# Kernel optimization log

Hardware: AMD Instinct MI355X
Metric: run time of the kernel (lower is better)

The kernel has to match this reference:

```python
import jax, jax.numpy as jnp
import numpy as np

N = 100000
E = 1600000
K = 15        # kernel_size (num Gaussian mixture components)
DIM = 3       # pseudo-coordinate dim
EPS = 1e-15   # PyG GMMConv sigma epsilon
BN_EPS = 1e-5
CH = [(50, 75), (75, 100), (100, 75), (75, 50)]


def setup_inputs() -> dict:
    key = jax.random.key(0)
    ks = iter(jax.random.split(key, 64))
    inp = {}
    inp["x"] = jax.random.normal(next(ks), (N, 50), jnp.float32)
    inp["edge_index"] = jax.random.randint(next(ks), (2, E), 0, N, jnp.int64)
    inp["edge_attr"] = jax.random.uniform(next(ks), (E, DIM), jnp.float32)
    for l, (cin, cout) in enumerate(CH, 1):
        inp[f"g{l}"] = jax.random.normal(next(ks), (cin, K, cout), jnp.float32) * 0.1
        inp[f"mu{l}"] = jax.random.normal(next(ks), (K, DIM), jnp.float32)
        inp[f"sigma{l}"] = jnp.ones((K, DIM), jnp.float32) + 0.1 * jax.random.uniform(next(ks), (K, DIM), jnp.float32)
        inp[f"root{l}"] = jax.random.normal(next(ks), (cin, cout), jnp.float32) * 0.1
        inp[f"b{l}"] = jax.random.normal(next(ks), (cout,), jnp.float32) * 0.01
        if l < 4:
            inp[f"gamma{l}"] = jnp.ones((cout,), jnp.float32)
            inp[f"beta{l}"] = jnp.zeros((cout,), jnp.float32)
    return inp


def gmm_layer(x, src, tgt, pseudo, g, mu, sigma, root, bias):
    # Gaussian mixture edge weights: w[e,k] = exp(-0.5 * sum_d (u_ed - mu_kd)^2 / sigma_kd^2)
    n = x.shape[0]
    diff = pseudo[:, None, :] - mu[None, :, :]              # [E,K,dim]
    w = jnp.exp(-0.5 * jnp.sum(diff * diff / (sigma[None] ** 2 + EPS), axis=-1))  # [E,K]
    xs = x[src]                                             # gather source feats [E,Cin]
    # out_t = sum_k (sum_{e->t} w_ek * x_src[e]) @ G_k  (avoids [E,K,Cout] tensor)
    agg = jnp.zeros((n, g.shape[2]), x.dtype)
    for k in range(K):
        zk = jax.ops.segment_sum(xs * w[:, k:k + 1], tgt, num_segments=n)  # [N,Cin]
        agg = agg + zk @ g[:, k, :]
    deg = jax.ops.segment_sum(jnp.ones((src.shape[0],), x.dtype), tgt, num_segments=n)
    agg = agg / jnp.maximum(deg, 1.0)[:, None]              # aggr='mean'
    return agg + x @ root + bias


def batchnorm(x, gamma, beta):
    m = jnp.mean(x, axis=0)
    v = jnp.var(x, axis=0)
    return gamma * (x - m) * jax.lax.rsqrt(v + BN_EPS) + beta


def reference(x, edge_index, edge_attr,
              g1, mu1, sigma1, root1, b1, gamma1, beta1,
              g2, mu2, sigma2, root2, b2, gamma2, beta2,
              g3, mu3, sigma3, root3, b3, gamma3, beta3,
              g4, mu4, sigma4, root4, b4):
    src, tgt = edge_index[0], edge_index[1]
    h = jax.nn.elu(gmm_layer(x, src, tgt, edge_attr, g1, mu1, sigma1, root1, b1))
    h = batchnorm(h, gamma1, beta1)
    h = jax.nn.elu(gmm_layer(h, src, tgt, edge_attr, g2, mu2, sigma2, root2, b2))
    h = batchnorm(h, gamma2, beta2)
    h = jax.nn.elu(gmm_layer(h, src, tgt, edge_attr, g3, mu3, sigma3, root3, b3))
    h = batchnorm(h, gamma3, beta3)
    return gmm_layer(h, src, tgt, edge_attr, g4, mu4, sigma4, root4, b4)
```

## Files before the change

kernel.cpp:

```cpp
#include <hip/hip_runtime.h>
#include <stdint.h>

#define NN 100000
#define NE 1600000
#define KG 15

typedef unsigned short u16;
typedef __attribute__((ext_vector_type(8))) short short8;
typedef __attribute__((ext_vector_type(4))) short short4_t;
typedef __attribute__((ext_vector_type(8))) __bf16 bf16x8;
typedef __attribute__((ext_vector_type(4))) float f32x4;

#ifdef __has_builtin
# if __has_builtin(__builtin_amdgcn_mfma_f32_16x16x16bf16_1k)
#  define HAS_MFMA16 1
# endif
#endif
#ifndef HAS_MFMA16
# define HAS_MFMA16 0
#endif

static __device__ __forceinline__ float bf2f(u16 u){ return __uint_as_float(((unsigned)u)<<16); }
static __device__ __forceinline__ u16 f2bf(float f){
  unsigned u = __float_as_uint(f);
  u += 0x7FFFu + ((u>>16)&1u);
  return (u16)(u>>16);
}
static __device__ __forceinline__ float ldf(const void* p, long long i, int isf32){
  return isf32 ? ((const float*)p)[i] : bf2f(((const u16*)p)[i]);
}
static __device__ __forceinline__ int ld_idx(const void* p, long long i, int isi64){
  return isi64 ? (int)((const long long*)p)[i] : ((const int*)p)[i];
}
static __device__ __forceinline__ f32x4 mfma16x16x32(short8 a, short8 b, f32x4 c){
  return __builtin_amdgcn_mfma_f32_16x16x32_bf16(
      __builtin_bit_cast(bf16x8, a), __builtin_bit_cast(bf16x8, b), c, 0, 0, 0);
}
#if HAS_MFMA16
static __device__ __forceinline__ f32x4 mfma16x16x16(short4_t a, short4_t b, f32x4 c){
  return __builtin_amdgcn_mfma_f32_16x16x16bf16_1k(a, b, c, 0, 0, 0);
}
#endif

__global__ void k_sentinel(float* out, float val){
  if (threadIdx.x == 0 && blockIdx.x == 0) out[0] = val;
}

__global__ void k_probe(const void* sg1, const void* ei, int* flags){
  if (threadIdx.x == 0 && blockIdx.x == 0){
    const u16* p = (const u16*)sg1;
    int sane = 1;
    for (int i=0;i<45;i++){ float v = bf2f(p[i]); if (!(v > 0.5f && v < 2.0f)) sane = 0; }
    flags[0] = sane ? 0 : 1;
    const int* q = (const int*)ei;
    int allz = 1;
    for (int i=1;i<128;i+=2) if (q[i] != 0) allz = 0;
    flags[1] = allz ? 1 : 0;
  }
}

__global__ __launch_bounds__(256) void k_convx(const void* x, u16* xcv, const int* flags){
  int i = blockIdx.x*256 + threadIdx.x;
  int c = i & 63, r = i >> 6;
  if (r >= NN) return;
  int isf = flags[0];
  u16 v = 0;
  if (c < 50){
    long long s = (long long)r*50 + c;
    v = isf ? f2bf(((const float*)x)[s]) : ((const u16*)x)[s];
  }
  xcv[(size_t)r*64 + c] = v;
}

__global__ __launch_bounds__(256) void k_deg(const void* ei, int* __restrict__ deg, const int* flags){
  int e = blockIdx.x*256 + threadIdx.x;
  int isi64 = flags[1];
  atomicAdd(&deg[ld_idx(ei, (long long)NE + e, isi64)], 1);
}

__global__ __launch_bounds__(256) void k_scan1(const int* __restrict__ deg, int* __restrict__ rp,
                                               int* __restrict__ bsum){
  __shared__ int lds[256];
  int b = blockIdx.x, t = threadIdx.x;
  int base = b*1024 + t*4;
  int v[4]; int s = 0;
  #pragma unroll
  for (int i=0;i<4;i++){ v[i] = (base+i < NN) ? deg[base+i] : 0; s += v[i]; }
  lds[t] = s; __syncthreads();
  int inc = s;
  for (int off=1; off<256; off<<=1){
    int y = (t>=off) ? lds[t-off] : 0;
    __syncthreads();
    inc += y; lds[t] = inc;
    __syncthreads();
  }
  int excl = inc - s;
  #pragma unroll
  for (int i=0;i<4;i++){ if (base+i < NN) rp[base+i] = excl; excl += v[i]; }
  if (t == 255) bsum[b] = inc;
}

__global__ __launch_bounds__(128) void k_scan2(int* __restrict__ bsum, int* __restrict__ rp){
  __shared__ int lds[128];
  int t = threadIdx.x;
  const int nb = (NN + 1023)/1024;
  int s = (t < nb) ? bsum[t] : 0;
  lds[t] = s; __syncthreads();
  int inc = s;
  for (int off=1; off<128; off<<=1){
    int y = (t>=off) ? lds[t-off] : 0;
    __syncthreads();
    inc += y; lds[t] = inc;
    __syncthreads();
  }
  bsum[t] = inc - s;
  if (t == 0) rp[NN] = NE;
}

__global__ __launch_bounds__(256) void k_scan3(int* __restrict__ rp, const int* __restrict__ bsum){
  int b = blockIdx.x, t = threadIdx.x;
  int add = bsum[b];
  int base = b*1024 + t*4;
  #pragma unroll
  for (int i=0;i<4;i++) if (base+i < NN) rp[base+i] += add;
}

__global__ __launch_bounds__(256) void k_fill(const void* ei, const void* attr,
                                              const int* __restrict__ rp, int* __restrict__ cur,
                                              int* __restrict__ perm, int4* __restrict__ csr16,
                                              int emode, const int* flags){
  int e = blockIdx.x*256 + threadIdx.x;
  int isf = flags[0], isi64 = flags[1];
  int t = ld_idx(ei, (long long)NE + e, isi64);
  int p = rp[t] + atomicAdd(&cur[t], 1);
  if (emode){
    int s = ld_idx(ei, e, isi64);
    float u0 = ldf(attr, 3LL*e+0, isf), u1 = ldf(attr, 3LL*e+1, isf), u2 = ldf(attr, 3LL*e+2, isf);
    csr16[p] = make_int4(s, __float_as_int(u0), __float_as_int(u1), __float_as_int(u2));
  } else {
    perm[p] = e;
  }
}

__global__ __launch_bounds__(256) void k_repack(const void* g, const void* root,
                                                u16* __restrict__ bp, int KC, int CIN, int COUT,
                                                int KS, int NCT, const int* flags){
  int tid = blockIdx.x*256 + threadIdx.x;
  int total = NCT*KS*64;
  if (tid >= total) return;
  int isf = flags[0];
  int lane = tid & 63;
  int ks = (tid >> 6) % KS;
  int ct = tid / (64*KS);
  int c = ct*16 + (lane & 15);
  int kbase = ks*32 + (lane >> 4)*8;
  short8 v8 = {};
  #pragma unroll
  for (int j=0;j<8;j++){
    int kk = kbase + j; u16 v = 0;
    if (c < COUT){
      if (kk < KC){
        int k = kk / CIN, cin = kk - k*CIN;
        v = f2bf(ldf(g, ((long long)cin*KG + k)*COUT + c, isf));
      } else if (kk < KC + CIN){
        v = f2bf(ldf(root, (long long)(kk-KC)*COUT + c, isf));
      }
    }
    v8[j] = (short)v;
  }
  ((short8*)bp)[tid] = v8;
}

template<int CIN, int COUT, int KPAD, int NCT, int XS, bool EM16, bool FINAL>
__global__ __launch_bounds__(512) void k_fused(
    const int4* __restrict__ csr16, const int* __restrict__ perm,
    const void* ei, const void* attr, const int* __restrict__ rp,
    const u16* __restrict__ xin, const void* mu, const void* sg,
    const u16* __restrict__ bp, const void* bias,
    u16* __restrict__ h, float* __restrict__ outp,
    float* __restrict__ sums, float* __restrict__ sumsq, const int* flags)
{
  constexpr int KC   = CIN*KG;
  constexpr int P    = (CIN + 31)/32;
  constexpr int NA   = 2*P;
  constexpr int RS   = KPAD + 8;
  constexpr int KS   = KPAD/32;
  __shared__ short8 zsh[16*RS/8];
  u16* zb = (u16*)zsh;

  int isf = flags[0], isi64 = flags[1];
  int wv = threadIdx.x >> 6, lane = threadIdx.x & 63;
  int m = lane & 15, q = lane >> 4;
  int node0 = blockIdx.x * 16;

  bool kvalid = (m < KG);
  int mm = kvalid ? m : 0;
  float mu0 = ldf(mu, mm*3+0, isf), mu1 = ldf(mu, mm*3+1, isf), mu2 = ldf(mu, mm*3+2, isf);
  float s0 = ldf(sg, mm*3+0, isf),  s1 = ldf(sg, mm*3+1, isf),  s2 = ldf(sg, mm*3+2, isf);
  float is0 = 1.f/(s0*s0 + 1e-15f), is1 = 1.f/(s1*s1 + 1e-15f), is2 = 1.f/(s2*s2 + 1e-15f);

  #pragma unroll 1
  for (int s = 0; s < 2; s++){
    int r = wv*2 + s;
    int t = node0 + r;
    int rs = rp[t], re = rp[t+1];
    f32x4 acc[NA] = {};
    int lastE = re - 1;
    int dg = re - rs;

#if HAS_MFMA16
    if (EM16 && dg >= 1 && dg <= 16){
      int e0 = rs + q*4;
      int4 ce[4];
      #pragma unroll
      for (int j=0;j<4;j++){
        int ep = e0 + j; ep = (ep > lastE) ? lastE : ep;
        ce[j] = csr16[ep];
      }
      int srcs[4];
      #pragma unroll
      for (int j=0;j<4;j++) srcs[j] = ce[j].x;
      unsigned xw[4*P];
      #pragma unroll
      for (int p=0; p<P; p++)
        #pragma unroll
        for (int j=0;j<4;j++)
          xw[p*4+j] = *(const unsigned*)(xin + (size_t)srcs[j]*XS + p*32 + 2*m);
      short4_t af4;
      #pragma unroll
      for (int j=0;j<4;j++){
        float u0 = __int_as_float(ce[j].y), u1 = __int_as_float(ce[j].z), u2 = __int_as_float(ce[j].w);
        float d0 = u0 - mu0, d1 = u1 - mu1, d2 = u2 - mu2;
        float w = __expf(-0.5f*(d0*d0*is0 + d1*d1*is1 + d2*d2*is2));
        bool ok = kvalid && (e0 + j <= lastE);
        af4[j] = (short)(ok ? f2bf(w) : (u16)0);
      }
      #pragma unroll
      for (int p=0; p<P; p++){
        int cin_e = p*32 + 2*m;
        bool ve = (cin_e < CIN), vo = (cin_e + 1 < CIN);
        short4_t bfe, bfo;
        #pragma unroll
        for (int j=0;j<4;j++){
          bfe[j] = ve ? (short)(xw[p*4+j] & 0xffffu) : (short)0;
          bfo[j] = vo ? (short)(xw[p*4+j] >> 16) : (short)0;
        }
        acc[2*p]   = mfma16x16x16(af4, bfe, acc[2*p]);
        acc[2*p+1] = mfma16x16x16(af4, bfo, acc[2*p+1]);
      }
    } else
#endif
    {
      for (int base = rs; base < re; base += 32){
        int e0 = base + q*8;
        int srcs[8];
        float u0[8], u1[8], u2[8];
        if (EM16){
          int4 ce[8];
          #pragma unroll
          for (int j=0;j<8;j++){
            int ep = e0 + j; ep = (ep > lastE) ? lastE : ep;
            ce[j] = csr16[ep];
          }
          #pragma unroll
          for (int j=0;j<8;j++){
            srcs[j] = ce[j].x;
            u0[j] = __int_as_float(ce[j].y); u1[j] = __int_as_float(ce[j].z); u2[j] = __int_as_float(ce[j].w);
          }
        } else {
          int eix[8];
          #pragma unroll
          for (int j=0;j<8;j++){
            int ep = e0 + j; ep = (ep > lastE) ? lastE : ep;
            eix[j] = perm[ep];
          }
          #pragma unroll
          for (int j=0;j<8;j++) srcs[j] = ld_idx(ei, eix[j], isi64);
          #pragma unroll
          for (int j=0;j<8;j++){
            u0[j] = ldf(attr, 3LL*eix[j]+0, isf);
            u1[j] = ldf(attr, 3LL*eix[j]+1, isf);
            u2[j] = ldf(attr, 3LL*eix[j]+2, isf);
          }
        }

        unsigned xw[8*P];
        #pragma unroll
        for (int p=0; p<P; p++)
          #pragma unroll
          for (int j=0;j<8;j++)
            xw[p*8+j] = *(const unsigned*)(xin + (size_t)srcs[j]*XS + p*32 + 2*m);

        short8 af;
        #pragma unroll
        for (int j=0;j<8;j++){
          float d0 = u0[j] - mu0, d1 = u1[j] - mu1, d2 = u2[j] - mu2;
          float w = __expf(-0.5f*(d0*d0*is0 + d1*d1*is1 + d2*d2*is2));
          bool ok = kvalid && (e0 + j <= lastE);
          w = ok ? w : 0.f;
          af[j] = (short)f2bf(w);
        }

        #pragma unroll
        for (int p=0; p<P; p++){
          int cin_e = p*32 + 2*m;
          bool ve = (cin_e < CIN), vo = (cin_e + 1 < CIN);
          short8 bfe, bfo;
          #pragma unroll
          for (int j=0;j<8;j++){
            bfe[j] = ve ? (short)(xw[p*8+j] & 0xffffu) : (short)0;
            bfo[j] = vo ? (short)(xw[p*8+j] >> 16) : (short)0;
          }
          acc[2*p]   = mfma16x16x32(af, bfe, acc[2*p]);
          acc[2*p+1] = mfma16x16x32(af, bfo, acc[2*p+1]);
        }
      }
    }

    float inv = 1.f / (float)(dg > 0 ? dg : 1);
    u16* row = zb + r*RS;
    #pragma unroll
    for (int ct=0; ct<NA; ct++){
      int cin = (ct>>1)*32 + 2*m + (ct&1);
      if (cin < CIN){
        #pragma unroll
        for (int rr=0;rr<4;rr++){
          int k = q*4 + rr;
          if (k < KG) row[k*CIN + cin] = f2bf(acc[ct][rr]*inv);
        }
      }
    }
    for (int idx = lane; idx < KPAD - KC; idx += 64){
      u16 v = 0;
      if (idx < CIN) v = xin[(size_t)t*XS + idx];
      row[KC + idx] = v;
    }
  }

  __syncthreads();

  if (wv < NCT){
    const short8* bpv = (const short8*)bp;
    const short8* zv  = (const short8*)zsh;
    f32x4 a0 = {}, a1 = {};
    #pragma unroll 2
    for (int ks=0; ks+1<KS; ks+=2){
      short8 af0 = zv[m*(RS/8) + ks*4 + q];
      short8 bf0 = bpv[(wv*KS + ks)*64 + lane];
      a0 = mfma16x16x32(af0, bf0, a0);
      short8 af1 = zv[m*(RS/8) + (ks+1)*4 + q];
      short8 bf1 = bpv[(wv*KS + ks+1)*64 + lane];
      a1 = mfma16x16x32(af1, bf1, a1);
    }
    if (KS & 1){
      short8 af0 = zv[m*(RS/8) + (KS-1)*4 + q];
      short8 bf0 = bpv[(wv*KS + KS-1)*64 + lane];
      a0 = mfma16x16x32(af0, bf0, a0);
    }
    f32x4 acc = a0 + a1;
    int col = wv*16 + m;
    if (col < COUT){
      float bv = ldf(bias, col, isf);
      float vs[4];
      #pragma unroll
      for (int rr=0;rr<4;rr++){
        int rrow = node0 + q*4 + rr;
        float v = acc[rr] + bv;
        if (!FINAL){
          v = (v > 0.f) ? v : (__expf(v) - 1.f);
          vs[rr] = v;
          h[(size_t)rrow*COUT + col] = f2bf(v);
        } else {
          outp[(size_t)rrow*COUT + col] = v;
        }
      }
      if (!FINAL){
        float ss = vs[0]+vs[1]+vs[2]+vs[3];
        float qq = vs[0]*vs[0]+vs[1]*vs[1]+vs[2]*vs[2]+vs[3]*vs[3];
        ss += __shfl_xor(ss, 16); ss += __shfl_xor(ss, 32);
        qq += __shfl_xor(qq, 16); qq += __shfl_xor(qq, 32);
        if (q == 0){
          atomicAdd(&sums[col], ss);
          atomicAdd(&sumsq[col], qq);
        }
      }
    }
  }
}

__global__ __launch_bounds__(256) void k_bn(const u16* __restrict__ h, const void* gamma,
                                            const void* beta, const float* __restrict__ sums,
                                            const float* __restrict__ sumsq, u16* __restrict__ xo,
                                            int COUT, const int* flags){
  int t = threadIdx.x;
  int isf = flags[0];
  int c = t & 127;
  int r = blockIdx.x*2 + (t >> 7);
  if (r >= NN) return;
  if (c >= COUT){
    if (c < 128) xo[(size_t)r*128 + c] = 0;
    return;
  }
  const float invn = 1.f/(float)NN;
  float mean = sums[c]*invn;
  float var  = sumsq[c]*invn - mean*mean;
  float g = ldf(gamma, c, isf), b = ldf(beta, c, isf);
  float v = g*(bf2f(h[(size_t)r*COUT + c]) - mean)*rsqrtf(var + 1e-5f) + b;
  xo[(size_t)r*128 + c] = f2bf(v);
}

extern "C" void kernel_launch(void* const* d_in, const int* in_sizes, int n_in,
                              void* d_out, int out_size, void* d_ws, size_t ws_size,
                              hipStream_t stream)
{
  static const int expected[29] = {
    5000000, 3200000, 4800000,
    56250, 45, 45, 3750, 75, 75, 75,
    112500, 45, 45, 7500, 100, 100, 100,
    112500, 45, 45, 7500, 75, 75, 75,
    56250, 45, 45, 3750, 50
  };
  if (n_in != 29){ k_sentinel<<<1, 64, 0, stream>>>((float*)d_out, 512.0f); return; }
  for (int j=0;j<29;j++){
    if (in_sizes[j] != expected[j]){
      k_sentinel<<<1, 64, 0, stream>>>((float*)d_out, 1024.0f*(float)(1+j));
      return;
    }
  }

  const void* x0   = d_in[0];
  const void* ei   = d_in[1];
  const void* attr = d_in[2];
  const void* G[4]  = {d_in[3],  d_in[10], d_in[17], d_in[24]};
  const void* MU[4] = {d_in[4],  d_in[11], d_in[18], d_in[25]};
  const void* SG[4] = {d_in[5],  d_in[12], d_in[19], d_in[26]};
  const void* RT[4] = {d_in[6],  d_in[13], d_in[20], d_in[27]};
  const void* BI[4] = {d_in[7],  d_in[14], d_in[21], d_in[28]};
  const void* GA[3] = {d_in[8],  d_in[15], d_in[22]};
  const void* BE[3] = {d_in[9],  d_in[16], d_in[23]};

  char* w = (char*)d_ws;
  auto alloc = [&](size_t bytes)->char*{ char* p = w; w += (bytes + 255) & ~(size_t)255; return p; };
  int*  flags = (int*) alloc(256);
  int*  deg  = (int*) alloc((size_t)NN*4);
  int*  cur  = (int*) alloc((size_t)NN*4);
  int*  rp   = (int*) alloc((size_t)(NN+1)*4);
  int*  bsum = (int*) alloc(512*4);
  u16*  h    = (u16*) alloc((size_t)NN*100*2);
  u16*  xb   = (u16*) alloc((size_t)NN*128*2);
  u16*  bp   = (u16*) alloc(1<<19);
  float* sums  = (float*)alloc(512);
  float* sumsq = (float*)alloc(512);
  u16*  xcv  = xb + (size_t)NN*64;

  size_t base = (size_t)(w - (char*)d_ws);
  int emode; int* perm = nullptr; int4* csr16 = nullptr;
  if (ws_size >= base + (size_t)NE*16 + 4096){
    emode = 1; csr16 = (int4*)alloc((size_t)NE*16);
  } else if (ws_size >= base + (size_t)NE*4 + 4096){
    emode = 0; perm = (int*)alloc((size_t)NE*4);
  } else {
    float mb = (float)(ws_size >> 20); if (mb > 255.f) mb = 255.f;
    k_sentinel<<<1, 64, 0, stream>>>((float*)d_out, 65536.0f + 256.0f*mb);
    return;
  }

  k_probe<<<1, 64, 0, stream>>>(SG[0], ei, flags);
  k_convx<<<NN*64/256, 256, 0, stream>>>(x0, xcv, flags);

  hipMemsetAsync(deg, 0, (size_t)NN*4, stream);
  hipMemsetAsync(cur, 0, (size_t)NN*4, stream);
  k_deg  <<<NE/256, 256, 0, stream>>>(ei, deg, flags);
  k_scan1<<<(NN+1023)/1024, 256, 0, stream>>>(deg, rp, bsum);
  k_scan2<<<1, 128, 0, stream>>>(bsum, rp);
  k_scan3<<<(NN+1023)/1024, 256, 0, stream>>>(rp, bsum);
  k_fill <<<NE/256, 256, 0, stream>>>(ei, attr, rp, cur, perm, csr16, emode, flags);

  const int NB = NN/16;

  {
    k_repack<<<(5*25*64 + 255)/256, 256, 0, stream>>>(G[0], RT[0], bp, 750, 50, 75, 25, 5, flags);
    hipMemsetAsync(sums, 0, 512, stream); hipMemsetAsync(sumsq, 0, 512, stream);
    if (emode) k_fused<50,75,800,5,64,true ,false><<<NB,512,0,stream>>>(csr16, perm, ei, attr, rp, xcv, MU[0], SG[0], bp, BI[0], h, nullptr, sums, sumsq, flags);
    else       k_fused<50,75,800,5,64,false,false><<<NB,512,0,stream>>>(csr16, perm, ei, attr, rp, xcv, MU[0], SG[0], bp, BI[0], h, nullptr, sums, sumsq, flags);
    k_bn<<<NN/2, 256, 0, stream>>>(h, GA[0], BE[0], sums, sumsq, xb, 75, flags);
  }

  {
    k_repack<<<(7*38*64 + 255)/256, 256, 0, stream>>>(G[1], RT[1], bp, 1125, 75, 100, 38, 7, flags);
    hipMemsetAsync(sums, 0, 512, stream); hipMemsetAsync(sumsq, 0, 512, stream);
    if (emode) k_fused<75,100,1216,7,128,true ,false><<<NB,512,0,stream>>>(csr16, perm, ei, attr, rp, xb, MU[1], SG[1], bp, BI[1], h, nullptr, sums, sumsq, flags);
    else       k_fused<75,100,1216,7,128,false,false><<<NB,512,0,stream>>>(csr16, perm, ei, attr, rp, xb, MU[1], SG[1], bp, BI[1], h, nullptr, sums, sumsq, flags);
    k_bn<<<NN/2, 256, 0, stream>>>(h, GA[1], BE[1], sums, sumsq, xb, 100, flags);
  }

  {
    k_repack<<<(5*50*64 + 255)/256, 256, 0, stream>>>(G[2], RT[2], bp, 1500, 100, 75, 50, 5, flags);
    hipMemsetAsync(sums, 0, 512, stream); hipMemsetAsync(sumsq, 0, 512, stream);
    if (emode) k_fused<100,75,1600,5,128,true ,false><<<NB,512,0,stream>>>(csr16, perm, ei, attr, rp, xb, MU[2], SG[2], bp, BI[2], h, nullptr, sums, sumsq, flags);
    else       k_fused<100,75,1600,5,128,false,false><<<NB,512,0,stream>>>(csr16, perm, ei, attr, rp, xb, MU[2], SG[2], bp, BI[2], h, nullptr, sums, sumsq, flags);
    k_bn<<<NN/2, 256, 0, stream>>>(h, GA[2], BE[2], sums, sumsq, xb, 75, flags);
  }

  {
    k_repack<<<(4*38*64 + 255)/256, 256, 0, stream>>>(G[3], RT[3], bp, 1125, 75, 50, 38, 4, flags);
    if (emode) k_fused<75,50,1216,4,128,true ,true><<<NB,512,0,stream>>>(csr16, perm, ei, attr, rp, xb, MU[3], SG[3], bp, BI[3], nullptr, (float*)d_out, sums, sumsq, flags);
    else       k_fused<75,50,1216,4,128,false,true><<<NB,512,0,stream>>>(csr16, perm, ei, attr, rp, xb, MU[3], SG[3], bp, BI[3], nullptr, (float*)d_out, sums, sumsq, flags);
  }
}
```

Before: 1.057 ms.

## Process nodes in degree-sorted order to balance work within fused blocks

Adds a counting sort of nodes by in-degree (histogram, scan, scatter) and makes each fused-layer block process 16 nodes of similar degree via an order array, writing outputs through an LDS node-id table. The aim is to cut load imbalance between waves in a block, where a high-degree node stalls its neighbours, and to group nodes so the small-degree fast path is taken uniformly. In exchange, stores to h and the output become scattered rows instead of contiguous ones, and three small preprocessing kernels are added.

```diff
diff --git a/kernel.cpp b/kernel.cpp
--- a/kernel.cpp
+++ b/kernel.cpp
@@ -140,6 +140,37 @@
   } else {
     perm[p] = e;
   }
+}
+
+__global__ __launch_bounds__(256) void k_hist(const int* __restrict__ deg, int* __restrict__ hist){
+  int i = blockIdx.x*256 + threadIdx.x;
+  if (i >= NN) return;
+  int d = deg[i]; if (d > 255) d = 255;
+  atomicAdd(&hist[255 - d], 1);
+}
+
+__global__ __launch_bounds__(256) void k_hscan(int* __restrict__ hist){
+  __shared__ int lds[256];
+  int t = threadIdx.x;
+  int v = hist[t];
+  lds[t] = v; __syncthreads();
+  int inc = v;
+  for (int off=1; off<256; off<<=1){
+    int y = (t>=off) ? lds[t-off] : 0;
+    __syncthreads();
+    inc += y; lds[t] = inc;
+    __syncthreads();
+  }
+  hist[t] = inc - v;
+}
+
+__global__ __launch_bounds__(256) void k_order(const int* __restrict__ deg, int* __restrict__ hist,
+                                               int* __restrict__ order){
+  int i = blockIdx.x*256 + threadIdx.x;
+  if (i >= NN) return;
+  int d = deg[i]; if (d > 255) d = 255;
+  int pos = atomicAdd(&hist[255 - d], 1);
+  order[pos] = i;
 }
 
 __global__ __launch_bounds__(256) void k_repack(const void* g, const void* root,
@@ -175,6 +206,7 @@
 __global__ __launch_bounds__(512) void k_fused(
     const int4* __restrict__ csr16, const int* __restrict__ perm,
     const void* ei, const void* attr, const int* __restrict__ rp,
+    const int* __restrict__ order,
     const u16* __restrict__ xin, const void* mu, const void* sg,
     const u16* __restrict__ bp, const void* bias,
     u16* __restrict__ h, float* __restrict__ outp,
@@ -186,6 +218,7 @@
   constexpr int RS   = KPAD + 8;
   constexpr int KS   = KPAD/32;
   __shared__ short8 zsh[16*RS/8];
+  __shared__ int nid[16];
   u16* zb = (u16*)zsh;
 
   int isf = flags[0], isi64 = flags[1];
@@ -202,7 +235,8 @@
   #pragma unroll 1
   for (int s = 0; s < 2; s++){
     int r = wv*2 + s;
-    int t = node0 + r;
+    int t = order[node0 + r];
+    if (lane == 0) nid[r] = t;
     int rs = rp[t], re = rp[t+1];
     f32x4 acc[NA] = {};
     int lastE = re - 1;
@@ -364,7 +398,7 @@
       float vs[4];
       #pragma unroll
       for (int rr=0;rr<4;rr++){
-        int rrow = node0 + q*4 + rr;
+        int rrow = nid[q*4 + rr];
         float v = acc[rr] + bv;
         if (!FINAL){
           v = (v > 0.f) ? v : (__expf(v) - 1.f);
@@ -446,6 +480,8 @@
   int*  cur  = (int*) alloc((size_t)NN*4);
   int*  rp   = (int*) alloc((size_t)(NN+1)*4);
   int*  bsum = (int*) alloc(512*4);
+  int*  hist = (int*) alloc(256*4);
+  int*  order= (int*) alloc((size_t)NN*4);
   u16*  h    = (u16*) alloc((size_t)NN*100*2);
   u16*  xb   = (u16*) alloc((size_t)NN*128*2);
   u16*  bp   = (u16*) alloc(1<<19);
@@ -470,41 +506,45 @@
 
   hipMemsetAsync(deg, 0, (size_t)NN*4, stream);
   hipMemsetAsync(cur, 0, (size_t)NN*4, stream);
+  hipMemsetAsync(hist, 0, 256*4, stream);
   k_deg  <<<NE/256, 256, 0, stream>>>(ei, deg, flags);
   k_scan1<<<(NN+1023)/1024, 256, 0, stream>>>(deg, rp, bsum);
   k_scan2<<<1, 128, 0, stream>>>(bsum, rp);
   k_scan3<<<(NN+1023)/1024, 256, 0, stream>>>(rp, bsum);
   k_fill <<<NE/256, 256, 0, stream>>>(ei, attr, rp, cur, perm, csr16, emode, flags);
+  k_hist <<<(NN+255)/256, 256, 0, stream>>>(deg, hist);
+  k_hscan<<<1, 256, 0, stream>>>(hist);
+  k_order<<<(NN+255)/256, 256, 0, stream>>>(deg, hist, order);
 
   const int NB = NN/16;
 
   {
     k_repack<<<(5*25*64 + 255)/256, 256, 0, stream>>>(G[0], RT[0], bp, 750, 50, 75, 25, 5, flags);
     hipMemsetAsync(sums, 0, 512, stream); hipMemsetAsync(sumsq, 0, 512, stream);
-    if (emode) k_fused<50,75,800,5,64,true ,false><<<NB,512,0,stream>>>(csr16, perm, ei, attr, rp, xcv, MU[0], SG[0], bp, BI[0], h, nullptr, sums, sumsq, flags);
-    else       k_fused<50,75,800,5,64,false,false><<<NB,512,0,stream>>>(csr16, perm, ei, attr, rp, xcv, MU[0], SG[0], bp, BI[0], h, nullptr, sums, sumsq, flags);
+    if (emode) k_fused<50,75,800,5,64,true ,false><<<NB,512,0,stream>>>(csr16, perm, ei, attr, rp, order, xcv, MU[0], SG[0], bp, BI[0], h, nullptr, sums, sumsq, flags);
+    else       k_fused<50,75,800,5,64,false,false><<<NB,512,0,stream>>>(csr16, perm, ei, attr, rp, order, xcv, MU[0], SG[0], bp, BI[0], h, nullptr, sums, sumsq, flags);
     k_bn<<<NN/2, 256, 0, stream>>>(h, GA[0], BE[0], sums, sumsq, xb, 75, flags);
   }
 
   {
     k_repack<<<(7*38*64 + 255)/256, 256, 0, stream>>>(G[1], RT[1], bp, 1125, 75, 100, 38, 7, flags);
     hipMemsetAsync(sums, 0, 512, stream); hipMemsetAsync(sumsq, 0, 512, stream);
-    if (emode) k_fused<75,100,1216,7,128,true ,false><<<NB,512,0,stream>>>(csr16, perm, ei, attr, rp, xb, MU[1], SG[1], bp, BI[1], h, nullptr, sums, sumsq, flags);
-    else       k_fused<75,100,1216,7,128,false,false><<<NB,512,0,stream>>>(csr16, perm, ei, attr, rp, xb, MU[1], SG[1], bp, BI[1], h, nullptr, sums, sumsq, flags);
+    if (emode) k_fused<75,100,1216,7,128,true ,false><<<NB,512,0,stream>>>(csr16, perm, ei, attr, rp, order, xb, MU[1], SG[1], bp, BI[1], h, nullptr, sums, sumsq, flags);
+    else       k_fused<75,100,1216,7,128,false,false><<<NB,512,0,stream>>>(csr16, perm, ei, attr, rp, order, xb, MU[1], SG[1], bp, BI[1], h, nullptr, sums, sumsq, flags);
     k_bn<<<NN/2, 256, 0, stream>>>(h, GA[1], BE[1], sums, sumsq, xb, 100, flags);
   }
 
   {
     k_repack<<<(5*50*64 + 255)/256, 256, 0, stream>>>(G[2], RT[2], bp, 1500, 100, 75, 50, 5, flags);
     hipMemsetAsync(sums, 0, 512, stream); hipMemsetAsync(sumsq, 0, 512, stream);
-    if (emode) k_fused<100,75,1600,5,128,true ,false><<<NB,512,0,stream>>>(csr16, perm, ei, attr, rp, xb, MU[2], SG[2], bp, BI[2], h, nullptr, sums, sumsq, flags);
-    else       k_fused<100,75,1600,5,128,false,false><<<NB,512,0,stream>>>(csr16, perm, ei, attr, rp, xb, MU[2], SG[2], bp, BI[2], h, nullptr, sums, sumsq, flags);
+    if (emode) k_fused<100,75,1600,5,128,true ,false><<<NB,512,0,stream>>>(csr16, perm, ei, attr, rp, order, xb, MU[2], SG[2], bp, BI[2], h, nullptr, sums, sumsq, flags);
+    else       k_fused<100,75,1600,5,128,false,false><<<NB,512,0,stream>>>(csr16, perm, ei, attr, rp, order, xb, MU[2], SG[2], bp, BI[2], h, nullptr, sums, sumsq, flags);
     k_bn<<<NN/2, 256, 0, stream>>>(h, GA[2], BE[2], sums, sumsq, xb, 75, flags);
   }
 
   {
     k_repack<<<(4*38*64 + 255)/256, 256, 0, stream>>>(G[3], RT[3], bp, 1125, 75, 50, 38, 4, flags);
-    if (emode) k_fused<75,50,1216,4,128,true ,true><<<NB,512,0,stream>>>(csr16, perm, ei, attr, rp, xb, MU[3], SG[3], bp, BI[3], nullptr, (float*)d_out, sums, sumsq, flags);
-    else       k_fused<75,50,1216,4,128,false,true><<<NB,512,0,stream>>>(csr16, perm, ei, attr, rp, xb, MU[3], SG[3], bp, BI[3], nullptr, (float*)d_out, sums, sumsq, flags);
-  }
-}
+    if (emode) k_fused<75,50,1216,4,128,true ,true><<<NB,512,0,stream>>>(csr16, perm, ei, attr, rp, order, xb, MU[3], SG[3], bp, BI[3], nullptr, (float*)d_out, sums, sumsq, flags);
+    else       k_fused<75,50,1216,4,128,false,true><<<NB,512,0,stream>>>(csr16, perm, ei, attr, rp, order, xb, MU[3], SG[3], bp, BI[3], nullptr, (float*)d_out, sums, sumsq, flags);
+  }
+}
```

New measurement: 1.606 ms. 51.9% more time.

## Fold batchnorm affine into next layer weights, drop separate BN kernels

Applied to the files above, without the earlier changes.

Removes the standalone batchnorm pass by folding the per-channel scale into the next layer's mixture and root weights during repack. The shift is carried by an extra constant-one input channel that the fused kernel writes into the padded activation buffer. Layers now write ELU output directly into 128-stride bf16 buffers that alternate between two ping-pong copies, with separate stat accumulators per layer. This saves three full read/write passes over the node features, at the cost of one extra input channel per layer and a slower repack that loops over channels for the bias row.

```diff
diff --git a/kernel.cpp b/kernel.cpp
--- a/kernel.cpp
+++ b/kernel.cpp
@@ -143,8 +143,12 @@
 }
 
 __global__ __launch_bounds__(256) void k_repack(const void* g, const void* root,
-                                                u16* __restrict__ bp, int KC, int CIN, int COUT,
-                                                int KS, int NCT, const int* flags){
+                                                const void* gamma, const void* beta,
+                                                const float* __restrict__ sums,
+                                                const float* __restrict__ sumsq,
+                                                u16* __restrict__ bp, int KC, int CIN, int CINp,
+                                                int COUT, int KS, int NCT, int fold,
+                                                const int* flags){
   int tid = blockIdx.x*256 + threadIdx.x;
   int total = NCT*KS*64;
   if (tid >= total) return;
@@ -154,6 +158,7 @@
   int ct = tid / (64*KS);
   int c = ct*16 + (lane & 15);
   int kbase = ks*32 + (lane >> 4)*8;
+  const float invn = 1.f/(float)NN;
   short8 v8 = {};
   #pragma unroll
   for (int j=0;j<8;j++){
@@ -161,9 +166,44 @@
     if (c < COUT){
       if (kk < KC){
         int k = kk / CIN, cin = kk - k*CIN;
-        v = f2bf(ldf(g, ((long long)cin*KG + k)*COUT + c, isf));
+        if (!fold){
+          v = f2bf(ldf(g, ((long long)cin*KG + k)*COUT + c, isf));
+        } else if (cin < CINp){
+          float mean = sums[cin]*invn;
+          float var  = sumsq[cin]*invn - mean*mean;
+          float a = ldf(gamma, cin, isf)*rsqrtf(var + 1e-5f);
+          v = f2bf(a * ldf(g, ((long long)cin*KG + k)*COUT + c, isf));
+        } else {
+          float s = 0.f;
+          for (int c2=0;c2<CINp;c2++){
+            float mean = sums[c2]*invn;
+            float var  = sumsq[c2]*invn - mean*mean;
+            float a = ldf(gamma, c2, isf)*rsqrtf(var + 1e-5f);
+            float b = ldf(beta, c2, isf) - mean*a;
+            s += b * ldf(g, ((long long)c2*KG + k)*COUT + c, isf);
+          }
+          v = f2bf(s);
+        }
       } else if (kk < KC + CIN){
-        v = f2bf(ldf(root, (long long)(kk-KC)*COUT + c, isf));
+        int r2 = kk - KC;
+        if (!fold){
+          v = f2bf(ldf(root, (long long)r2*COUT + c, isf));
+        } else if (r2 < CINp){
+          float mean = sums[r2]*invn;
+          float var  = sumsq[r2]*invn - mean*mean;
+          float a = ldf(gamma, r2, isf)*rsqrtf(var + 1e-5f);
+          v = f2bf(a * ldf(root, (long long)r2*COUT + c, isf));
+        } else {
+          float s = 0.f;
+          for (int c2=0;c2<CINp;c2++){
+            float mean = sums[c2]*invn;
+            float var  = sumsq[c2]*invn - mean*mean;
+            float a = ldf(gamma, c2, isf)*rsqrtf(var + 1e-5f);
+            float b = ldf(beta, c2, isf) - mean*a;
+            s += b * ldf(root, (long long)c2*COUT + c, isf);
+          }
+          v = f2bf(s);
+        }
       }
     }
     v8[j] = (short)v;
@@ -177,7 +217,7 @@
     const void* ei, const void* attr, const int* __restrict__ rp,
     const u16* __restrict__ xin, const void* mu, const void* sg,
     const u16* __restrict__ bp, const void* bias,
-    u16* __restrict__ h, float* __restrict__ outp,
+    u16* __restrict__ xo, float* __restrict__ outp,
     float* __restrict__ sums, float* __restrict__ sumsq, const int* flags)
 {
   constexpr int KC   = CIN*KG;
@@ -369,7 +409,7 @@
         if (!FINAL){
           v = (v > 0.f) ? v : (__expf(v) - 1.f);
           vs[rr] = v;
-          h[(size_t)rrow*COUT + col] = f2bf(v);
+          xo[(size_t)rrow*128 + col] = f2bf(v);
         } else {
           outp[(size_t)rrow*COUT + col] = v;
         }
@@ -386,27 +426,9 @@
       }
     }
   }
-}
-
-__global__ __launch_bounds__(256) void k_bn(const u16* __restrict__ h, const void* gamma,
-                                            const void* beta, const float* __restrict__ sums,
-                                            const float* __restrict__ sumsq, u16* __restrict__ xo,
-                                            int COUT, const int* flags){
-  int t = threadIdx.x;
-  int isf = flags[0];
-  int c = t & 127;
-  int r = blockIdx.x*2 + (t >> 7);
-  if (r >= NN) return;
-  if (c >= COUT){
-    if (c < 128) xo[(size_t)r*128 + c] = 0;
-    return;
-  }
-  const float invn = 1.f/(float)NN;
-  float mean = sums[c]*invn;
-  float var  = sumsq[c]*invn - mean*mean;
-  float g = ldf(gamma, c, isf), b = ldf(beta, c, isf);
-  float v = g*(bf2f(h[(size_t)r*COUT + c]) - mean)*rsqrtf(var + 1e-5f) + b;
-  xo[(size_t)r*128 + c] = f2bf(v);
+  if (!FINAL){
+    if (wv == 0 && lane < 16) xo[(size_t)(node0 + lane)*128 + COUT] = (u16)0x3F80;
+  }
 }
 
 extern "C" void kernel_launch(void* const* d_in, const int* in_sizes, int n_in,
@@ -446,12 +468,13 @@
   int*  cur  = (int*) alloc((size_t)NN*4);
   int*  rp   = (int*) alloc((size_t)(NN+1)*4);
   int*  bsum = (int*) alloc(512*4);
-  u16*  h    = (u16*) alloc((size_t)NN*100*2);
-  u16*  xb   = (u16*) alloc((size_t)NN*128*2);
+  u16*  xbA  = (u16*) alloc((size_t)NN*128*2);
+  u16*  xbB  = (u16*) alloc((size_t)NN*128*2);
   u16*  bp   = (u16*) alloc(1<<19);
-  float* sums  = (float*)alloc(512);
-  float* sumsq = (float*)alloc(512);
-  u16*  xcv  = xb + (size_t)NN*64;
+  float* sums1 = (float*)alloc(512); float* sumsq1 = (float*)alloc(512);
+  float* sums2 = (float*)alloc(512); float* sumsq2 = (float*)alloc(512);
+  float* sums3 = (float*)alloc(512); float* sumsq3 = (float*)alloc(512);
+  u16*  xcv  = xbB;
 
   size_t base = (size_t)(w - (char*)d_ws);
   int emode; int* perm = nullptr; int4* csr16 = nullptr;
@@ -470,6 +493,9 @@
 
   hipMemsetAsync(deg, 0, (size_t)NN*4, stream);
   hipMemsetAsync(cur, 0, (size_t)NN*4, stream);
+  hipMemsetAsync(sums1, 0, 512, stream); hipMemsetAsync(sumsq1, 0, 512, stream);
+  hipMemsetAsync(sums2, 0, 512, stream); hipMemsetAsync(sumsq2, 0, 512, stream);
+  hipMemsetAsync(sums3, 0, 512, stream); hipMemsetAsync(sumsq3, 0, 512, stream);
   k_deg  <<<NE/256, 256, 0, stream>>>(ei, deg, flags);
   k_scan1<<<(NN+1023)/1024, 256, 0, stream>>>(deg, rp, bsum);
   k_scan2<<<1, 128, 0, stream>>>(bsum, rp);
@@ -479,32 +505,30 @@
   const int NB = NN/16;
 
   {
-    k_repack<<<(5*25*64 + 255)/256, 256, 0, stream>>>(G[0], RT[0], bp, 750, 50, 75, 25, 5, flags);
-    hipMemsetAsync(sums, 0, 512, stream); hipMemsetAsync(sumsq, 0, 512, stream);
-    if (emode) k_fused<50,75,800,5,64,true ,false><<<NB,512,0,stream>>>(csr16, perm, ei, attr, rp, xcv, MU[0], SG[0], bp, BI[0], h, nullptr, sums, sumsq, flags);
-    else       k_fused<50,75,800,5,64,false,false><<<NB,512,0,stream>>>(csr16, perm, ei, attr, rp, xcv, MU[0], SG[0], bp, BI[0], h, nullptr, sums, sumsq, flags);
-    k_bn<<<NN/2, 256, 0, stream>>>(h, GA[0], BE[0], sums, sumsq, xb, 75, flags);
+    k_repack<<<(5*25*64 + 255)/256, 256, 0, stream>>>(G[0], RT[0], GA[0], BE[0], sums1, sumsq1,
+                                                      bp, 750, 50, 50, 75, 25, 5, 0, flags);
+    if (emode) k_fused<50,75,800,5,64,true ,false><<<NB,512,0,stream>>>(csr16, perm, ei, attr, rp, xcv, MU[0], SG[0], bp, BI[0], xbA, nullptr, sums1, sumsq1, flags);
+    else       k_fused<50,75,800,5,64,false,false><<<NB,512,0,stream>>>(csr16, perm, ei, attr, rp, xcv, MU[0], SG[0], bp, BI[0], xbA, nullptr, sums1, sumsq1, flags);
   }
 
   {
-    k_repack<<<(7*38*64 + 255)/256, 256, 0, stream>>>(G[1], RT[1], bp, 1125, 75, 100, 38, 7, flags);
-    hipMemsetAsync(sums, 0, 512, stream); hipMemsetAsync(sumsq, 0, 512, stream);
-    if (emode) k_fused<75,100,1216,7,128,true ,false><<<NB,512,0,stream>>>(csr16, perm, ei, attr, rp, xb, MU[1], SG[1], bp, BI[1], h, nullptr, sums, sumsq, flags);
-    else       k_fused<75,100,1216,7,128,false,false><<<NB,512,0,stream>>>(csr16, perm, ei, attr, rp, xb, MU[1], SG[1], bp, BI[1], h, nullptr, sums, sumsq, flags);
-    k_bn<<<NN/2, 256, 0, stream>>>(h, GA[1], BE[1], sums, sumsq, xb, 100, flags);
+    k_repack<<<(7*38*64 + 255)/256, 256, 0, stream>>>(G[1], RT[1], GA[0], BE[0], sums1, sumsq1,
+                                                      bp, 1140, 76, 75, 100, 38, 7, 1, flags);
+    if (emode) k_fused<76,100,1216,7,128,true ,false><<<NB,512,0,stream>>>(csr16, perm, ei, attr, rp, xbA, MU[1], SG[1], bp, BI[1], xbB, nullptr, sums2, sumsq2, flags);
+    else       k_fused<76,100,1216,7,128,false,false><<<NB,512,0,stream>>>(csr16, perm, ei, attr, rp, xbA, MU[1], SG[1], bp, BI[1], xbB, nullptr, sums2, sumsq2, flags);
   }
 
   {
-    k_repack<<<(5*50*64 + 255)/256, 256, 0, stream>>>(G[2], RT[2], bp, 1500, 100, 75, 50, 5, flags);
-    hipMemsetAsync(sums, 0, 512, stream); hipMemsetAsync(sumsq, 0, 512, stream);
-    if (emode) k_fused<100,75,1600,5,128,true ,false><<<NB,512,0,stream>>>(csr16, perm, ei, attr, rp, xb, MU[2], SG[2], bp, BI[2], h, nullptr, sums, sumsq, flags);
-    else       k_fused<100,75,1600,5,128,false,false><<<NB,512,0,stream>>>(csr16, perm, ei, attr, rp, xb, MU[2], SG[2], bp, BI[2], h, nullptr, sums, sumsq, flags);
-    k_bn<<<NN/2, 256, 0, stream>>>(h, GA[2], BE[2], sums, sumsq, xb, 75, flags);
+    k_repack<<<(5*51*64 + 255)/256, 256, 0, stream>>>(G[2], RT[2], GA[1], BE[1], sums2, sumsq2,
+                                                      bp, 1515, 101, 100, 75, 51, 5, 1, flags);
+    if (emode) k_fused<101,75,1632,5,128,true ,false><<<NB,512,0,stream>>>(csr16, perm, ei, attr, rp, xbB, MU[2], SG[2], bp, BI[2], xbA, nullptr, sums3, sumsq3, flags);
+    else       k_fused<101,75,1632,5,128,false,false><<<NB,512,0,stream>>>(csr16, perm, ei, attr, rp, xbB, MU[2], SG[2], bp, BI[2], xbA, nullptr, sums3, sumsq3, flags);
   }
 
   {
-    k_repack<<<(4*38*64 + 255)/256, 256, 0, stream>>>(G[3], RT[3], bp, 1125, 75, 50, 38, 4, flags);
-    if (emode) k_fused<75,50,1216,4,128,true ,true><<<NB,512,0,stream>>>(csr16, perm, ei, attr, rp, xb, MU[3], SG[3], bp, BI[3], nullptr, (float*)d_out, sums, sumsq, flags);
-    else       k_fused<75,50,1216,4,128,false,true><<<NB,512,0,stream>>>(csr16, perm, ei, attr, rp, xb, MU[3], SG[3], bp, BI[3], nullptr, (float*)d_out, sums, sumsq, flags);
-  }
-}
+    k_repack<<<(4*38*64 + 255)/256, 256, 0, stream>>>(G[3], RT[3], GA[2], BE[2], sums3, sumsq3,
+                                                      bp, 1140, 76, 75, 50, 38, 4, 1, flags);
+    if (emode) k_fused<76,50,1216,4,128,true ,true><<<NB,512,0,stream>>>(csr16, perm, ei, attr, rp, xbA, MU[3], SG[3], bp, BI[3], nullptr, (float*)d_out, sums3, sumsq3, flags);
+    else       k_fused<76,50,1216,4,128,false,true><<<NB,512,0,stream>>>(csr16, perm, ei, attr, rp, xbA, MU[3], SG[3], bp, BI[3], nullptr, (float*)d_out, sums3, sumsq3, flags);
+  }
+}
```

Result: no change. 1.073 ms (+1.5%).
